# Performance work log

Hardware: AMD Instinct MI355X
Metric: run time of the kernel (lower is better)

Reference implementation:

```python
import jax, jax.numpy as jnp
import numpy as np

N_NODES = 50000
N_NEIB = 64
D = 256
BATCH = 1024
N_SAMPLES = (25, 10)  # fanout per layer (layer_specs n_sample)


def setup_inputs() -> dict:
    key = jax.random.key(0)
    ks = jax.random.split(key, 12)
    inp = {
        'ids': jax.random.randint(ks[0], (BATCH,), 0, N_NODES),
        'diff_idx': jax.random.randint(ks[1], (N_NODES, N_NEIB), 0, N_NODES),
        'diff_val': jax.random.uniform(ks[2], (N_NODES, N_NEIB), dtype=jnp.float32),
        'feats': jax.random.normal(ks[3], (N_NODES, D), dtype=jnp.float32),
    }
    # two aggregator layers, each: fc_x, fc_neib : D -> D (= output_dim//2)
    for li in range(2):
        inp[f'Wx{li+1}'] = jax.random.normal(ks[4 + 4 * li], (D, D), dtype=jnp.float32) * 0.05
        inp[f'bx{li+1}'] = jnp.zeros((D,), dtype=jnp.float32)
        inp[f'Wn{li+1}'] = jax.random.normal(ks[5 + 4 * li], (D, D), dtype=jnp.float32) * 0.05
        inp[f'bn{li+1}'] = jnp.zeros((D,), dtype=jnp.float32)
    return inp


def _sample(diff_idx, diff_val, ids, n_samples, key):
    # gather candidate neighbor rows, shared random column permutation, take first n_samples
    tmp_idx = diff_idx[ids]            # [n, N_NEIB]
    tmp_val = diff_val[ids]
    perm = jax.random.permutation(key, tmp_idx.shape[1])
    idx = tmp_idx[:, perm][:, :n_samples].reshape(-1)
    val = tmp_val[:, perm][:, :n_samples].reshape(-1)
    return idx, val


def _agg(x, neib, vals, Wx, bx, Wn, bn):
    # weighted-mean neighbor aggregation + self/neib linear combine + relu
    n = x.shape[0]
    d = neib.shape[1]
    neib = neib.reshape(n, -1, d)              # [n, s, d]
    vals = vals.reshape(n, -1)                 # [n, s]
    w = vals / (jnp.sum(vals, axis=1, keepdims=True) + 1e-10)
    m = jnp.einsum('nsd,ns->nd', neib, w)      # weighted mean of neighbors
    return jax.nn.relu(x @ Wx + bx + m @ Wn + bn)


def reference(ids, diff_idx, diff_val, feats,
              Wx1, bx1, Wn1, bn1, Wx2, bx2, Wn2, bn2):
    skey = jax.random.key(42)
    all_feats = [feats[ids]]
    all_vals = []
    cur = ids
    for li, n in enumerate(N_SAMPLES):
        cur, vals = _sample(diff_idx, diff_val, cur, n, jax.random.fold_in(skey, li))
        all_feats.append(feats[cur])
        all_vals.append(vals)
    params = [(Wx1, bx1, Wn1, bn1), (Wx2, bx2, Wn2, bn2)]
    for Wx, bx, Wn, bn in params:
        all_feats = [_agg(all_feats[k], all_feats[k + 1], all_vals[k], Wx, bx, Wn, bn)
                     for k in range(len(all_feats) - 1)]
    assert len(all_feats) == 1
    return all_feats[0]  # [BATCH, D]
```

## Files before the change

kernel.cpp:

```cpp
#include <hip/hip_runtime.h>
#include <stdint.h>
#include <stddef.h>
#include <algorithm>

#define BATCH  1024
#define S1     25
#define S2     10
#define DIM    256
#define NNEIB  64
#define L2ROWS (BATCH * S1)
#define MROWS  (BATCH + BATCH * S1)
#define KTOT   512

struct Perm25 { int p[S1]; };
struct Perm10 { int p[S2]; };

typedef __attribute__((ext_vector_type(8))) short short8;
typedef __attribute__((ext_vector_type(4))) float f32x4;

static inline uint32_t rotl_(uint32_t x, int d) { return (x << d) | (x >> (32 - d)); }

static void tf2x32(uint32_t k0, uint32_t k1, uint32_t x0, uint32_t x1,
                   uint32_t* o0, uint32_t* o1) {
  const uint32_t ks0 = k0, ks1 = k1, ks2 = k0 ^ k1 ^ 0x1BD11BDAu;
  static const int R[8] = {13, 15, 26, 6, 17, 29, 16, 24};
  x0 += ks0; x1 += ks1;
  for (int g = 0; g < 5; ++g) {
    const int* rr = R + (g & 1) * 4;
    for (int i = 0; i < 4; i++) { x0 += x1; x1 = rotl_(x1, rr[i]); x1 ^= x0; }
    uint32_t a, b;
    switch (g) {
      default:
      case 0: a = ks1; b = ks2; break;
      case 1: a = ks2; b = ks0; break;
      case 2: a = ks0; b = ks1; break;
      case 3: a = ks1; b = ks2; break;
      case 4: a = ks2; b = ks0; break;
    }
    x0 += a; x1 = x1 + b + (uint32_t)(g + 1);
  }
  *o0 = x0; *o1 = x1;
}

static void compute_perm(uint32_t li, int n, int* out) {
  uint32_t k0, k1, s0, s1;
  tf2x32(0u, 42u, 0u, li, &k0, &k1);
  tf2x32(k0, k1, 0u, 1u, &s0, &s1);
  uint32_t bits[NNEIB];
  for (int i = 0; i < NNEIB; i++) {
    uint32_t a, b;
    tf2x32(s0, s1, 0u, (uint32_t)i, &a, &b);
    bits[i] = a ^ b;
  }
  int idx[NNEIB];
  for (int i = 0; i < NNEIB; i++) idx[i] = i;
  std::stable_sort(idx, idx + NNEIB, [&](int A, int B) { return bits[A] < bits[B]; });
  for (int j = 0; j < n; j++) out[j] = idx[j];
}

__device__ __forceinline__ unsigned short f2bf(float x) {
  union { float f; uint32_t u; } v; v.f = x;
  uint32_t r = (v.u + 0x7FFFu + ((v.u >> 16) & 1u)) >> 16;
  return (unsigned short)r;
}
__device__ __forceinline__ float bf2f(unsigned short u) {
  union { uint32_t u; float f; } v; v.u = ((uint32_t)u) << 16;
  return v.f;
}


__global__ __launch_bounds__(256) void sample1_k(
    const int* __restrict__ ids, const int* __restrict__ dix,
    const float* __restrict__ dval, int* __restrict__ growB,
    float* __restrict__ w1, Perm25 pm) {
  int i = blockIdx.x * 256 + threadIdx.x;
  if (i >= BATCH) return;
  int nid = ids[i];
  growB[i] = nid;
  const float* vr = dval + (size_t)nid * NNEIB;
  const int* ir = dix + (size_t)nid * NNEIB;
  float v[S1];
  float s = 0.f;
  for (int j = 0; j < S1; j++) { v[j] = vr[pm.p[j]]; s += v[j]; }
  float inv = 1.f / (s + 1e-10f);
  for (int j = 0; j < S1; j++) {
    w1[i * S1 + j] = v[j] * inv;
    growB[BATCH + i * S1 + j] = ir[pm.p[j]];
  }
}

__global__ __launch_bounds__(256) void sample2_k(
    const int* __restrict__ idx1, const int* __restrict__ dix,
    const float* __restrict__ dval, int* __restrict__ idx2,
    float* __restrict__ w2, Perm10 pm) {
  int p = blockIdx.x * 256 + threadIdx.x;
  if (p >= L2ROWS) return;
  int nid = idx1[p];
  const float* vr = dval + (size_t)nid * NNEIB;
  const int* ir = dix + (size_t)nid * NNEIB;
  float v[S2];
  float s = 0.f;
  for (int j = 0; j < S2; j++) { v[j] = vr[pm.p[j]]; s += v[j]; }
  float inv = 1.f / (s + 1e-10f);
  for (int j = 0; j < S2; j++) {
    w2[p * S2 + j] = v[j] * inv;
    idx2[p * S2 + j] = ir[pm.p[j]];
  }
}

__global__ __launch_bounds__(256) void stage1_k(
    const float* __restrict__ feats, const int* __restrict__ growB,
    const int* __restrict__ idx1, const float* __restrict__ w1,
    const int* __restrict__ idx2, const float* __restrict__ w2,
    unsigned short* __restrict__ A1) {
  __shared__ int snbr[S1];
  __shared__ float sw[S1];
  int r = blockIdx.x, t = threadIdx.x;
  int s, base;
  const int* nb;
  const float* ww;
  if (r < BATCH) { s = S1; base = r * S1; nb = idx1; ww = w1; }
  else           { s = S2; base = (r - BATCH) * S2; nb = idx2; ww = w2; }
  if (t < s) { snbr[t] = nb[base + t]; sw[t] = ww[base + t]; }
  int xrow = growB[r];
  __syncthreads();
  float xv = feats[(size_t)xrow * DIM + t];
  float acc = 0.f;
  for (int j = 0; j < s; j++) acc += sw[j] * feats[(size_t)snbr[j] * DIM + t];
  A1[(size_t)r * KTOT + t]       = f2bf(xv);
  A1[(size_t)r * KTOT + DIM + t] = f2bf(acc);
}

__global__ __launch_bounds__(256) void stage2_k(
    const unsigned short* __restrict__ H, const float* __restrict__ w1,
    unsigned short* __restrict__ A2) {
  __shared__ float sw[S1];
  int i = blockIdx.x, t = threadIdx.x;
  if (t < S1) sw[t] = w1[i * S1 + t];
  __syncthreads();
  const unsigned short* hb = H + (size_t)(BATCH + i * S1) * DIM + t;
  float acc = 0.f;
  for (int j = 0; j < S1; j++) acc += sw[j] * bf2f(hb[(size_t)j * DIM]);
  A2[(size_t)i * KTOT + t]       = H[(size_t)i * DIM + t];
  A2[(size_t)i * KTOT + DIM + t] = f2bf(acc);
}

__global__ __launch_bounds__(256) void convw_k(
    const float* __restrict__ Wx, const float* __restrict__ Wn,
    unsigned short* __restrict__ Wt) {
  int idx = blockIdx.x * 256 + threadIdx.x;
  int n = idx >> 9;
  int k = idx & 511;
  float v = (k < DIM) ? Wx[(size_t)k * DIM + n] : Wn[(size_t)(k - DIM) * DIM + n];
  Wt[(size_t)n * KTOT + k] = f2bf(v);
}

#define BM 128
#define BN 64
#define BK 32
#define LPAD 40
template <bool OUT_BF16>
__global__ __launch_bounds__(256) void mfma_gemm_k(
    const unsigned short* __restrict__ A, const unsigned short* __restrict__ Wt,
    const float* __restrict__ bx, const float* __restrict__ bn,
    void* __restrict__ OutP, int M) {
  __shared__ __align__(16) unsigned short As[BM][LPAD];
  __shared__ __align__(16) unsigned short Bs[BN][LPAD];
  int t = threadIdx.x;
  int wave = t >> 6;
  int lane = t & 63;
  int quad = lane >> 4;
  int l16 = lane & 15;
  int row0 = blockIdx.x * BM;
  int col0 = blockIdx.y * BN;

  f32x4 acc[2][4];
#pragma unroll
  for (int i = 0; i < 2; i++)
#pragma unroll
    for (int j = 0; j < 4; j++) acc[i][j] = (f32x4){0.f, 0.f, 0.f, 0.f};

  int lr = t >> 2;
  int lq = (t & 3) * 8;

  for (int k0 = 0; k0 < KTOT; k0 += BK) {
    *(f32x4*)&As[lr][lq]      = *(const f32x4*)&A[(size_t)(row0 + lr) * KTOT + k0 + lq];
    *(f32x4*)&As[lr + 64][lq] = *(const f32x4*)&A[(size_t)(row0 + lr + 64) * KTOT + k0 + lq];
    *(f32x4*)&Bs[lr][lq]      = *(const f32x4*)&Wt[(size_t)(col0 + lr) * KTOT + k0 + lq];
    __syncthreads();

    short8 a0 = *(const short8*)&As[wave * 32 + l16][quad * 8];
    short8 a1 = *(const short8*)&As[wave * 32 + 16 + l16][quad * 8];
    short8 b0 = *(const short8*)&Bs[l16][quad * 8];
    short8 b1 = *(const short8*)&Bs[16 + l16][quad * 8];
    short8 b2 = *(const short8*)&Bs[32 + l16][quad * 8];
    short8 b3 = *(const short8*)&Bs[48 + l16][quad * 8];

    acc[0][0] = __builtin_amdgcn_mfma_f32_16x16x32_bf16(a0, b0, acc[0][0], 0, 0, 0);
    acc[0][1] = __builtin_amdgcn_mfma_f32_16x16x32_bf16(a0, b1, acc[0][1], 0, 0, 0);
    acc[0][2] = __builtin_amdgcn_mfma_f32_16x16x32_bf16(a0, b2, acc[0][2], 0, 0, 0);
    acc[0][3] = __builtin_amdgcn_mfma_f32_16x16x32_bf16(a0, b3, acc[0][3], 0, 0, 0);
    acc[1][0] = __builtin_amdgcn_mfma_f32_16x16x32_bf16(a1, b0, acc[1][0], 0, 0, 0);
    acc[1][1] = __builtin_amdgcn_mfma_f32_16x16x32_bf16(a1, b1, acc[1][1], 0, 0, 0);
    acc[1][2] = __builtin_amdgcn_mfma_f32_16x16x32_bf16(a1, b2, acc[1][2], 0, 0, 0);
    acc[1][3] = __builtin_amdgcn_mfma_f32_16x16x32_bf16(a1, b3, acc[1][3], 0, 0, 0);
    __syncthreads();
  }

#pragma unroll
  for (int j = 0; j < 4; j++) {
    int c = col0 + j * 16 + l16;
    float bias = bx[c] + bn[c];
#pragma unroll
    for (int i = 0; i < 2; i++) {
#pragma unroll
      for (int reg = 0; reg < 4; reg++) {
        int r = row0 + wave * 32 + i * 16 + quad * 4 + reg;
        float v = fmaxf(acc[i][j][reg] + bias, 0.f);
        if (OUT_BF16)
          ((unsigned short*)OutP)[(size_t)r * DIM + c] = f2bf(v);
        else
          ((float*)OutP)[(size_t)r * DIM + c] = v;
      }
    }
  }
}

static inline size_t align256(size_t x) { return (x + 255) & ~(size_t)255; }

extern "C" void kernel_launch(void* const* d_in, const int* in_sizes, int n_in,
                              void* d_out, int out_size, void* d_ws, size_t ws_size,
                              hipStream_t stream) {
  const int*   ids  = (const int*)d_in[0];
  const int*   dix  = (const int*)d_in[1];
  const float* dval = (const float*)d_in[2];
  const float* feats= (const float*)d_in[3];
  const float* Wx1  = (const float*)d_in[4];
  const float* bx1  = (const float*)d_in[5];
  const float* Wn1  = (const float*)d_in[6];
  const float* bn1  = (const float*)d_in[7];
  const float* Wx2  = (const float*)d_in[8];
  const float* bx2  = (const float*)d_in[9];
  const float* Wn2  = (const float*)d_in[10];
  const float* bn2  = (const float*)d_in[11];
  float* out = (float*)d_out;

  Perm25 p25;
  Perm10 p10;
  compute_perm(0u, S1, p25.p);
  compute_perm(1u, S2, p10.p);

  char* w = (char*)d_ws;
  int*            growB = (int*)w;            w += align256(sizeof(int) * MROWS);
  float*          w1    = (float*)w;          w += align256(sizeof(float) * L2ROWS);
  int*            idx2  = (int*)w;            w += align256(sizeof(int) * (size_t)L2ROWS * S2);
  float*          w2    = (float*)w;          w += align256(sizeof(float) * (size_t)L2ROWS * S2);
  unsigned short* A1    = (unsigned short*)w; w += align256(2 * (size_t)MROWS * KTOT);
  unsigned short* Hb    = (unsigned short*)w; w += align256(2 * (size_t)MROWS * DIM);
  unsigned short* A2    = (unsigned short*)w; w += align256(2 * (size_t)BATCH * KTOT);
  unsigned short* Wt1   = (unsigned short*)w; w += align256(2 * (size_t)DIM * KTOT);
  unsigned short* Wt2   = (unsigned short*)w; w += align256(2 * (size_t)DIM * KTOT);
  int* idx1 = growB + BATCH;

  convw_k<<<(DIM * KTOT) / 256, 256, 0, stream>>>(Wx1, Wn1, Wt1);
  convw_k<<<(DIM * KTOT) / 256, 256, 0, stream>>>(Wx2, Wn2, Wt2);
  sample1_k<<<(BATCH + 255) / 256, 256, 0, stream>>>(ids, dix, dval, growB, w1, p25);
  sample2_k<<<(L2ROWS + 255) / 256, 256, 0, stream>>>(idx1, dix, dval, idx2, w2, p10);
  stage1_k<<<MROWS, 256, 0, stream>>>(feats, growB, idx1, w1, idx2, w2, A1);
  mfma_gemm_k<true><<<dim3(MROWS / BM, DIM / BN), 256, 0, stream>>>(
      A1, Wt1, bx1, bn1, Hb, MROWS);
  stage2_k<<<BATCH, 256, 0, stream>>>(Hb, w1, A2);
  mfma_gemm_k<false><<<dim3(BATCH / BM, DIM / BN), 256, 0, stream>>>(
      A2, Wt2, bx2, bn2, out, BATCH);
}
```

Baseline: 210.6 us.

## Pre-convert features to bf16, use wave-per-row gathers, retile GEMMs

Adds a kernel that converts the whole 50000x256 fp32 feature table to bf16 so the neighbor gathers in stage1 read half the bytes. It also rewrites stage1 and stage2 so each wave handles one row: neighbor ids and weights are broadcast with shuffles and each lane does 8-byte vector loads. The GEMM is templated on tile size, using 128x128 tiles with a 2x2 wave layout for layer 1 and 64x64 tiles for layer 2. The risk is that converting the full table costs about 77 MB of traffic per call, while the gathers only touch roughly 260k rows, so the conversion may cost more than the gather savings.

```diff
diff --git a/kernel.cpp b/kernel.cpp
--- a/kernel.cpp
+++ b/kernel.cpp
@@ -11,6 +11,7 @@
 #define L2ROWS (BATCH * S1)
 #define MROWS  (BATCH + BATCH * S1)
 #define KTOT   512
+#define NFEAT  50000
 
 struct Perm25 { int p[S1]; };
 struct Perm10 { int p[S2]; };
@@ -63,11 +64,21 @@
   uint32_t r = (v.u + 0x7FFFu + ((v.u >> 16) & 1u)) >> 16;
   return (unsigned short)r;
 }
-__device__ __forceinline__ float bf2f(unsigned short u) {
-  union { uint32_t u; float f; } v; v.u = ((uint32_t)u) << 16;
+__device__ __forceinline__ float bfbits2f(uint32_t lo16) {
+  union { uint32_t u; float f; } v; v.u = lo16 << 16;
   return v.f;
 }
 
+
+__global__ __launch_bounds__(256) void convf_k(
+    const float* __restrict__ feats, uint32_t* __restrict__ fb) {
+  int i = blockIdx.x * 256 + threadIdx.x;
+  f32x4 v = *(const f32x4*)&feats[(size_t)i * 4];
+  uint32_t lo = f2bf(v.x) | ((uint32_t)f2bf(v.y) << 16);
+  uint32_t hi = f2bf(v.z) | ((uint32_t)f2bf(v.w) << 16);
+  fb[(size_t)i * 2]     = lo;
+  fb[(size_t)i * 2 + 1] = hi;
+}
 
 __global__ __launch_bounds__(256) void sample1_k(
     const int* __restrict__ ids, const int* __restrict__ dix,
@@ -109,40 +120,59 @@
 }
 
 __global__ __launch_bounds__(256) void stage1_k(
-    const float* __restrict__ feats, const int* __restrict__ growB,
+    const uint2* __restrict__ fb, const int* __restrict__ growB,
     const int* __restrict__ idx1, const float* __restrict__ w1,
     const int* __restrict__ idx2, const float* __restrict__ w2,
-    unsigned short* __restrict__ A1) {
-  __shared__ int snbr[S1];
-  __shared__ float sw[S1];
-  int r = blockIdx.x, t = threadIdx.x;
-  int s, base;
+    uint2* __restrict__ A1) {
+  int wave = threadIdx.x >> 6, lane = threadIdx.x & 63;
+  int r = blockIdx.x * 4 + wave;
+  int s;
   const int* nb;
   const float* ww;
-  if (r < BATCH) { s = S1; base = r * S1; nb = idx1; ww = w1; }
-  else           { s = S2; base = (r - BATCH) * S2; nb = idx2; ww = w2; }
-  if (t < s) { snbr[t] = nb[base + t]; sw[t] = ww[base + t]; }
+  if (r < BATCH) { s = S1; nb = idx1 + (size_t)r * S1; ww = w1 + (size_t)r * S1; }
+  else { s = S2; int b = r - BATCH; nb = idx2 + (size_t)b * S2; ww = w2 + (size_t)b * S2; }
+  int nbl = 0;
+  float wl = 0.f;
+  if (lane < s) { nbl = nb[lane]; wl = ww[lane]; }
   int xrow = growB[r];
-  __syncthreads();
-  float xv = feats[(size_t)xrow * DIM + t];
-  float acc = 0.f;
-  for (int j = 0; j < s; j++) acc += sw[j] * feats[(size_t)snbr[j] * DIM + t];
-  A1[(size_t)r * KTOT + t]       = f2bf(xv);
-  A1[(size_t)r * KTOT + DIM + t] = f2bf(acc);
+  A1[(size_t)r * 128 + lane] = fb[(size_t)xrow * 64 + lane];
+  float a0 = 0.f, a1 = 0.f, a2 = 0.f, a3 = 0.f;
+  for (int j = 0; j < s; j++) {
+    int nid = __shfl(nbl, j);
+    float wj = __shfl(wl, j);
+    uint2 u = fb[(size_t)nid * 64 + lane];
+    a0 += wj * bfbits2f(u.x & 0xffffu);
+    a1 += wj * bfbits2f(u.x >> 16);
+    a2 += wj * bfbits2f(u.y & 0xffffu);
+    a3 += wj * bfbits2f(u.y >> 16);
+  }
+  uint2 o;
+  o.x = f2bf(a0) | ((uint32_t)f2bf(a1) << 16);
+  o.y = f2bf(a2) | ((uint32_t)f2bf(a3) << 16);
+  A1[(size_t)r * 128 + 64 + lane] = o;
 }
 
 __global__ __launch_bounds__(256) void stage2_k(
-    const unsigned short* __restrict__ H, const float* __restrict__ w1,
-    unsigned short* __restrict__ A2) {
-  __shared__ float sw[S1];
-  int i = blockIdx.x, t = threadIdx.x;
-  if (t < S1) sw[t] = w1[i * S1 + t];
-  __syncthreads();
-  const unsigned short* hb = H + (size_t)(BATCH + i * S1) * DIM + t;
-  float acc = 0.f;
-  for (int j = 0; j < S1; j++) acc += sw[j] * bf2f(hb[(size_t)j * DIM]);
-  A2[(size_t)i * KTOT + t]       = H[(size_t)i * DIM + t];
-  A2[(size_t)i * KTOT + DIM + t] = f2bf(acc);
+    const uint2* __restrict__ Hb, const float* __restrict__ w1,
+    uint2* __restrict__ A2) {
+  int wave = threadIdx.x >> 6, lane = threadIdx.x & 63;
+  int i = blockIdx.x * 4 + wave;
+  float wl = (lane < S1) ? w1[(size_t)i * S1 + lane] : 0.f;
+  A2[(size_t)i * 128 + lane] = Hb[(size_t)i * 64 + lane];
+  const uint2* hb = Hb + (size_t)(BATCH + i * S1) * 64 + lane;
+  float a0 = 0.f, a1 = 0.f, a2 = 0.f, a3 = 0.f;
+  for (int j = 0; j < S1; j++) {
+    float wj = __shfl(wl, j);
+    uint2 u = hb[(size_t)j * 64];
+    a0 += wj * bfbits2f(u.x & 0xffffu);
+    a1 += wj * bfbits2f(u.x >> 16);
+    a2 += wj * bfbits2f(u.y & 0xffffu);
+    a3 += wj * bfbits2f(u.y >> 16);
+  }
+  uint2 o;
+  o.x = f2bf(a0) | ((uint32_t)f2bf(a1) << 16);
+  o.y = f2bf(a2) | ((uint32_t)f2bf(a3) << 16);
+  A2[(size_t)i * 128 + 64 + lane] = o;
 }
 
 __global__ __launch_bounds__(256) void convw_k(
@@ -155,68 +185,73 @@
   Wt[(size_t)n * KTOT + k] = f2bf(v);
 }
 
-#define BM 128
-#define BN 64
 #define BK 32
 #define LPAD 40
-template <bool OUT_BF16>
-__global__ __launch_bounds__(256) void mfma_gemm_k(
+template <int TBM, int TBN, bool OUT_BF16>
+__global__ __launch_bounds__(256) void gemm_k(
     const unsigned short* __restrict__ A, const unsigned short* __restrict__ Wt,
     const float* __restrict__ bx, const float* __restrict__ bn,
-    void* __restrict__ OutP, int M) {
-  __shared__ __align__(16) unsigned short As[BM][LPAD];
-  __shared__ __align__(16) unsigned short Bs[BN][LPAD];
+    void* __restrict__ OutP) {
+  constexpr int MI = TBM / 32;
+  constexpr int NJ = TBN / 32;
+  __shared__ __align__(16) unsigned short As[TBM][LPAD];
+  __shared__ __align__(16) unsigned short Bs[TBN][LPAD];
   int t = threadIdx.x;
-  int wave = t >> 6;
-  int lane = t & 63;
-  int quad = lane >> 4;
-  int l16 = lane & 15;
-  int row0 = blockIdx.x * BM;
-  int col0 = blockIdx.y * BN;
-
-  f32x4 acc[2][4];
-#pragma unroll
-  for (int i = 0; i < 2; i++)
-#pragma unroll
-    for (int j = 0; j < 4; j++) acc[i][j] = (f32x4){0.f, 0.f, 0.f, 0.f};
+  int wave = t >> 6, lane = t & 63, quad = lane >> 4, l16 = lane & 15;
+  int wm = (wave >> 1) * (TBM / 2);
+  int wn = (wave & 1) * (TBN / 2);
+  int row0 = blockIdx.x * TBM, col0 = blockIdx.y * TBN;
+
+  f32x4 acc[MI][NJ];
+#pragma unroll
+  for (int i = 0; i < MI; i++)
+#pragma unroll
+    for (int j = 0; j < NJ; j++) acc[i][j] = (f32x4){0.f, 0.f, 0.f, 0.f};
 
   int lr = t >> 2;
   int lq = (t & 3) * 8;
 
   for (int k0 = 0; k0 < KTOT; k0 += BK) {
-    *(f32x4*)&As[lr][lq]      = *(const f32x4*)&A[(size_t)(row0 + lr) * KTOT + k0 + lq];
-    *(f32x4*)&As[lr + 64][lq] = *(const f32x4*)&A[(size_t)(row0 + lr + 64) * KTOT + k0 + lq];
-    *(f32x4*)&Bs[lr][lq]      = *(const f32x4*)&Wt[(size_t)(col0 + lr) * KTOT + k0 + lq];
+#pragma unroll
+    for (int p = 0; p < TBM / 64; p++)
+      *(f32x4*)&As[p * 64 + lr][lq] =
+          *(const f32x4*)&A[(size_t)(row0 + p * 64 + lr) * KTOT + k0 + lq];
+#pragma unroll
+    for (int p = 0; p < TBN / 64; p++)
+      *(f32x4*)&Bs[p * 64 + lr][lq] =
+          *(const f32x4*)&Wt[(size_t)(col0 + p * 64 + lr) * KTOT + k0 + lq];
     __syncthreads();
 
-    short8 a0 = *(const short8*)&As[wave * 32 + l16][quad * 8];
-    short8 a1 = *(const short8*)&As[wave * 32 + 16 + l16][quad * 8];
-    short8 b0 = *(const short8*)&Bs[l16][quad * 8];
-    short8 b1 = *(const short8*)&Bs[16 + l16][quad * 8];
-    short8 b2 = *(const short8*)&Bs[32 + l16][quad * 8];
-    short8 b3 = *(const short8*)&Bs[48 + l16][quad * 8];
-
-    acc[0][0] = __builtin_amdgcn_mfma_f32_16x16x32_bf16(a0, b0, acc[0][0], 0, 0, 0);
-    acc[0][1] = __builtin_amdgcn_mfma_f32_16x16x32_bf16(a0, b1, acc[0][1], 0, 0, 0);
-    acc[0][2] = __builtin_amdgcn_mfma_f32_16x16x32_bf16(a0, b2, acc[0][2], 0, 0, 0);
-    acc[0][3] = __builtin_amdgcn_mfma_f32_16x16x32_bf16(a0, b3, acc[0][3], 0, 0, 0);
-    acc[1][0] = __builtin_amdgcn_mfma_f32_16x16x32_bf16(a1, b0, acc[1][0], 0, 0, 0);
-    acc[1][1] = __builtin_amdgcn_mfma_f32_16x16x32_bf16(a1, b1, acc[1][1], 0, 0, 0);
-    acc[1][2] = __builtin_amdgcn_mfma_f32_16x16x32_bf16(a1, b2, acc[1][2], 0, 0, 0);
-    acc[1][3] = __builtin_amdgcn_mfma_f32_16x16x32_bf16(a1, b3, acc[1][3], 0, 0, 0);
+    short8 af[MI], bfr[NJ];
+#pragma unroll
+    for (int i = 0; i < MI; i++)
+      af[i] = *(const short8*)&As[wm + i * 16 + l16][quad * 8];
+#pragma unroll
+    for (int j = 0; j < NJ; j++)
+      bfr[j] = *(const short8*)&Bs[wn + j * 16 + l16][quad * 8];
+#pragma unroll
+    for (int i = 0; i < MI; i++)
+#pragma unroll
+      for (int j = 0; j < NJ; j++)
+        acc[i][j] = __builtin_amdgcn_mfma_f32_16x16x32_bf16(af[i], bfr[j], acc[i][j], 0, 0, 0);
     __syncthreads();
   }
 
-#pragma unroll
-  for (int j = 0; j < 4; j++) {
-    int c = col0 + j * 16 + l16;
-    float bias = bx[c] + bn[c];
-#pragma unroll
-    for (int i = 0; i < 2; i++) {
+  float bias[NJ];
+#pragma unroll
+  for (int j = 0; j < NJ; j++) {
+    int c = col0 + wn + j * 16 + l16;
+    bias[j] = bx[c] + bn[c];
+  }
+#pragma unroll
+  for (int i = 0; i < MI; i++) {
+#pragma unroll
+    for (int j = 0; j < NJ; j++) {
+      int c = col0 + wn + j * 16 + l16;
 #pragma unroll
       for (int reg = 0; reg < 4; reg++) {
-        int r = row0 + wave * 32 + i * 16 + quad * 4 + reg;
-        float v = fmaxf(acc[i][j][reg] + bias, 0.f);
+        int r = row0 + wm + i * 16 + quad * 4 + reg;
+        float v = fmaxf(acc[i][j][reg] + bias[j], 0.f);
         if (OUT_BF16)
           ((unsigned short*)OutP)[(size_t)r * DIM + c] = f2bf(v);
         else
@@ -255,6 +290,7 @@
   float*          w1    = (float*)w;          w += align256(sizeof(float) * L2ROWS);
   int*            idx2  = (int*)w;            w += align256(sizeof(int) * (size_t)L2ROWS * S2);
   float*          w2    = (float*)w;          w += align256(sizeof(float) * (size_t)L2ROWS * S2);
+  uint32_t*       fb    = (uint32_t*)w;       w += align256(2 * (size_t)NFEAT * DIM);
   unsigned short* A1    = (unsigned short*)w; w += align256(2 * (size_t)MROWS * KTOT);
   unsigned short* Hb    = (unsigned short*)w; w += align256(2 * (size_t)MROWS * DIM);
   unsigned short* A2    = (unsigned short*)w; w += align256(2 * (size_t)BATCH * KTOT);
@@ -262,14 +298,16 @@
   unsigned short* Wt2   = (unsigned short*)w; w += align256(2 * (size_t)DIM * KTOT);
   int* idx1 = growB + BATCH;
 
+  convf_k<<<(NFEAT * DIM / 4) / 256, 256, 0, stream>>>(feats, fb);
   convw_k<<<(DIM * KTOT) / 256, 256, 0, stream>>>(Wx1, Wn1, Wt1);
   convw_k<<<(DIM * KTOT) / 256, 256, 0, stream>>>(Wx2, Wn2, Wt2);
   sample1_k<<<(BATCH + 255) / 256, 256, 0, stream>>>(ids, dix, dval, growB, w1, p25);
   sample2_k<<<(L2ROWS + 255) / 256, 256, 0, stream>>>(idx1, dix, dval, idx2, w2, p10);
-  stage1_k<<<MROWS, 256, 0, stream>>>(feats, growB, idx1, w1, idx2, w2, A1);
-  mfma_gemm_k<true><<<dim3(MROWS / BM, DIM / BN), 256, 0, stream>>>(
-      A1, Wt1, bx1, bn1, Hb, MROWS);
-  stage2_k<<<BATCH, 256, 0, stream>>>(Hb, w1, A2);
-  mfma_gemm_k<false><<<dim3(BATCH / BM, DIM / BN), 256, 0, stream>>>(
-      A2, Wt2, bx2, bn2, out, BATCH);
-}
+  stage1_k<<<MROWS / 4, 256, 0, stream>>>((const uint2*)fb, growB, idx1, w1, idx2, w2,
+                                          (uint2*)A1);
+  gemm_k<128, 128, true><<<dim3(MROWS / 128, DIM / 128), 256, 0, stream>>>(
+      A1, Wt1, bx1, bn1, Hb);
+  stage2_k<<<BATCH / 4, 256, 0, stream>>>((const uint2*)Hb, w1, (uint2*)A2);
+  gemm_k<64, 64, false><<<dim3(BATCH / 64, DIM / 64), 256, 0, stream>>>(
+      A2, Wt2, bx2, bn2, out);
+}
```

Result: faster. 202.2 us (-4.0%).
